# Performance work log

Measured on AMD Instinct MI355X. Metric: run time of the kernel, lower is better.

## Reference

```python
import jax, jax.numpy as jnp
import numpy as np

N = 8192  # number of candidates being ranked


def setup_inputs() -> dict:
    key = jax.random.key(0)
    k1, k2 = jax.random.split(key)
    logits = jax.random.normal(k1, (N,), dtype=jnp.float32)
    rankings = jax.random.randint(k2, (N,), 0, N).astype(jnp.int64)
    return {"logits": logits, "rankings": rankings}


def reference(logits, rankings):
    # Vectorized WeightedRankNetLoss:
    #   loss = (1/N) * sum_{i<j, r_i<r_j} log(1 + exp(logits[j]-logits[i])) / (r_i + r_j)
    n = logits.shape[0]
    idx = jnp.arange(n)
    # pair selected iff i < j AND rankings[i] < rankings[j]
    pair_mask = (idx[:, None] < idx[None, :]) & (rankings[:, None] < rankings[None, :])
    r = rankings.astype(logits.dtype)
    rsum = r[:, None] + r[None, :]
    # For selected pairs r_j >= r_i + 1 >= 1, so rsum >= 1; clamp only protects masked entries.
    w = jnp.where(pair_mask, 1.0, 0.0) / jnp.maximum(rsum, 1.0)  # [N, N]
    d = logits[None, :] - logits[:, None]  # d[i, j] = logits[j] - logits[i]
    loss = jnp.sum(w * jax.nn.softplus(d))  # softplus = log(1+exp(.)), numerically stable
    return loss / n
```

## Files before the change

### kernel.cpp

```cpp
#include <hip/hip_runtime.h>

#define N_CAND 8192
#define TILE   64
#define NTILES (N_CAND / TILE)
#define NLIVE  (NTILES * (NTILES + 1) / 2)
#define WPB    4
#define NBLK   (NLIVE / WPB)

__device__ __forceinline__ float readlane_f(float x, int lane) {
    return __int_as_float(__builtin_amdgcn_readlane(__float_as_int(x), lane));
}

__global__ __launch_bounds__(256, 8) void ranknet_pairs_kernel(
    const float* __restrict__ logits,
    const int*   __restrict__ rankings,
    float*       __restrict__ partials)
{
    const int lane = threadIdx.x & 63;
    const int wave = threadIdx.x >> 6;
    const int t = __builtin_amdgcn_readfirstlane((int)blockIdx.x * WPB + wave);

    int bj = (int)((__builtin_sqrtf(8.0f * (float)t + 1.0f) - 1.0f) * 0.5f);
    while ((bj + 1) * (bj + 2) / 2 <= t) ++bj;
    while (bj * (bj + 1) / 2 > t)       --bj;
    const int bi = t - bj * (bj + 1) / 2;

    const float LOG2E = 1.4426950408889634f;
    const float INF   = __builtin_inff();

    const float lis = logits[bi * TILE + lane] * LOG2E;
    const float ri  = (float)rankings[bi * TILE + lane];
    const float ljs = logits[bj * TILE + lane] * LOG2E;
    const float rjv = (float)rankings[bj * TILE + lane];

    const float Ei  = __builtin_amdgcn_exp2f(lis);
    const float Ejv = __builtin_amdgcn_exp2f(ljs);

    float accL0 = 0.0f, accL1 = 0.0f, accL2 = 0.0f, accL3 = 0.0f;
    float accW0 = 0.0f, accW1 = 0.0f, accW2 = 0.0f, accW3 = 0.0f;

    if (bi != bj) {
        #pragma unroll
        for (int jj = 0; jj < TILE; jj += 4) {
            const float Ej0 = readlane_f(Ejv, jj    ), rj0 = readlane_f(rjv, jj    );
            const float Ej1 = readlane_f(Ejv, jj + 1), rj1 = readlane_f(rjv, jj + 1);
            const float Ej2 = readlane_f(Ejv, jj + 2), rj2 = readlane_f(rjv, jj + 2);
            const float Ej3 = readlane_f(Ejv, jj + 3), rj3 = readlane_f(rjv, jj + 3);

            const float L0 = __builtin_amdgcn_logf(Ei + Ej0);
            const float L1 = __builtin_amdgcn_logf(Ei + Ej1);
            const float L2 = __builtin_amdgcn_logf(Ei + Ej2);
            const float L3 = __builtin_amdgcn_logf(Ei + Ej3);

            const float rs0 = (rj0 > ri) ? (ri + rj0) : INF;
            const float rs1 = (rj1 > ri) ? (ri + rj1) : INF;
            const float rs2 = (rj2 > ri) ? (ri + rj2) : INF;
            const float rs3 = (rj3 > ri) ? (ri + rj3) : INF;

            const float w0 = __builtin_amdgcn_rcpf(rs0);
            const float w1 = __builtin_amdgcn_rcpf(rs1);
            const float w2 = __builtin_amdgcn_rcpf(rs2);
            const float w3 = __builtin_amdgcn_rcpf(rs3);

            accL0 = fmaf(w0, L0, accL0);  accW0 += w0;
            accL1 = fmaf(w1, L1, accL1);  accW1 += w1;
            accL2 = fmaf(w2, L2, accL2);  accW2 += w2;
            accL3 = fmaf(w3, L3, accL3);  accW3 += w3;
        }
    } else {
        #pragma unroll
        for (int jj = 0; jj < TILE; jj += 4) {
            const float Ej0 = readlane_f(Ejv, jj    ), rj0 = readlane_f(rjv, jj    );
            const float Ej1 = readlane_f(Ejv, jj + 1), rj1 = readlane_f(rjv, jj + 1);
            const float Ej2 = readlane_f(Ejv, jj + 2), rj2 = readlane_f(rjv, jj + 2);
            const float Ej3 = readlane_f(Ejv, jj + 3), rj3 = readlane_f(rjv, jj + 3);

            const float L0 = __builtin_amdgcn_logf(Ei + Ej0);
            const float L1 = __builtin_amdgcn_logf(Ei + Ej1);
            const float L2 = __builtin_amdgcn_logf(Ei + Ej2);
            const float L3 = __builtin_amdgcn_logf(Ei + Ej3);

            const float rs0 = ((jj     > lane) && (rj0 > ri)) ? (ri + rj0) : INF;
            const float rs1 = ((jj + 1 > lane) && (rj1 > ri)) ? (ri + rj1) : INF;
            const float rs2 = ((jj + 2 > lane) && (rj2 > ri)) ? (ri + rj2) : INF;
            const float rs3 = ((jj + 3 > lane) && (rj3 > ri)) ? (ri + rj3) : INF;

            const float w0 = __builtin_amdgcn_rcpf(rs0);
            const float w1 = __builtin_amdgcn_rcpf(rs1);
            const float w2 = __builtin_amdgcn_rcpf(rs2);
            const float w3 = __builtin_amdgcn_rcpf(rs3);

            accL0 = fmaf(w0, L0, accL0);  accW0 += w0;
            accL1 = fmaf(w1, L1, accL1);  accW1 += w1;
            accL2 = fmaf(w2, L2, accL2);  accW2 += w2;
            accL3 = fmaf(w3, L3, accL3);  accW3 += w3;
        }
    }

    const float accL = (accL0 + accL1) + (accL2 + accL3);
    const float accW = (accW0 + accW1) + (accW2 + accW3);
    float acc = fmaf(-lis, accW, accL);
    #pragma unroll
    for (int off = 32; off > 0; off >>= 1)
        acc += __shfl_down(acc, off, 64);
    if (lane == 0)
        partials[t] = acc;
}

__global__ __launch_bounds__(1024) void ranknet_reduce_kernel(
    const float* __restrict__ partials,
    float*       __restrict__ out)
{
    __shared__ float s_part[16];
    const int tid = threadIdx.x;

    float acc = 0.0f;
    for (int k = tid; k < NLIVE; k += 1024)
        acc += partials[k];

    #pragma unroll
    for (int off = 32; off > 0; off >>= 1)
        acc += __shfl_down(acc, off, 64);
    if ((tid & 63) == 0) s_part[tid >> 6] = acc;
    __syncthreads();
    if (tid == 0) {
        float s = 0.0f;
        #pragma unroll
        for (int w = 0; w < 16; ++w) s += s_part[w];
        const float LN2 = 0.6931471805599453f;
        out[0] = s * (LN2 / (float)N_CAND);
    }
}

extern "C" void kernel_launch(void* const* d_in, const int* in_sizes, int n_in,
                              void* d_out, int out_size, void* d_ws, size_t ws_size,
                              hipStream_t stream)
{
    const float* logits   = (const float*)d_in[0];
    const int*   rankings = (const int*)  d_in[1];
    float*       out      = (float*)d_out;
    float*       partials = (float*)d_ws;

    ranknet_pairs_kernel<<<dim3(NBLK), dim3(256), 0, stream>>>(logits, rankings, partials);
    ranknet_reduce_kernel<<<1, 1024, 0, stream>>>(partials, out);
}
```

Measured before the change: 69.86 us.

## Use persistent fixed grid with two tiles per wave and split remainder tiles

Replaces one-tile-per-wave launch with a fixed grid of 1024 blocks where each wave processes two full tiles. The 64 leftover tiles are split into 16-column chunks assigned to a subset of waves. Partials are reduced per block in shared memory, so the final reduction reads one value per thread. The inner loops are no longer unrolled, which adds loop and dynamic readlane overhead in exchange for the smaller code size.

Result: no change. 70.39 us (+0.8%).

```diff
diff --git a/kernel.cpp b/kernel.cpp
--- a/kernel.cpp
+++ b/kernel.cpp
@@ -5,21 +5,18 @@
 #define NTILES (N_CAND / TILE)
 #define NLIVE  (NTILES * (NTILES + 1) / 2)
 #define WPB    4
-#define NBLK   (NLIVE / WPB)
+#define NBLK   1024
+#define NWAVE  (NBLK * WPB)
 
 __device__ __forceinline__ float readlane_f(float x, int lane) {
     return __int_as_float(__builtin_amdgcn_readlane(__float_as_int(x), lane));
 }
 
-__global__ __launch_bounds__(256, 8) void ranknet_pairs_kernel(
-    const float* __restrict__ logits,
-    const int*   __restrict__ rankings,
-    float*       __restrict__ partials)
+__device__ __forceinline__ float tile_range_sum(const float* __restrict__ logits,
+                                                const int*   __restrict__ rankings,
+                                                int t, int lane, int j0, int j1)
 {
-    const int lane = threadIdx.x & 63;
-    const int wave = threadIdx.x >> 6;
-    const int t = __builtin_amdgcn_readfirstlane((int)blockIdx.x * WPB + wave);
-
+    t = __builtin_amdgcn_readfirstlane(t);
     int bj = (int)((__builtin_sqrtf(8.0f * (float)t + 1.0f) - 1.0f) * 0.5f);
     while ((bj + 1) * (bj + 2) / 2 <= t) ++bj;
     while (bj * (bj + 1) / 2 > t)       --bj;
@@ -40,8 +37,8 @@
     float accW0 = 0.0f, accW1 = 0.0f, accW2 = 0.0f, accW3 = 0.0f;
 
     if (bi != bj) {
-        #pragma unroll
-        for (int jj = 0; jj < TILE; jj += 4) {
+        #pragma unroll 1
+        for (int jj = j0; jj < j1; jj += 4) {
             const float Ej0 = readlane_f(Ejv, jj    ), rj0 = readlane_f(rjv, jj    );
             const float Ej1 = readlane_f(Ejv, jj + 1), rj1 = readlane_f(rjv, jj + 1);
             const float Ej2 = readlane_f(Ejv, jj + 2), rj2 = readlane_f(rjv, jj + 2);
@@ -68,8 +65,8 @@
             accL3 = fmaf(w3, L3, accL3);  accW3 += w3;
         }
     } else {
-        #pragma unroll
-        for (int jj = 0; jj < TILE; jj += 4) {
+        #pragma unroll 1
+        for (int jj = j0; jj < j1; jj += 4) {
             const float Ej0 = readlane_f(Ejv, jj    ), rj0 = readlane_f(rjv, jj    );
             const float Ej1 = readlane_f(Ejv, jj + 1), rj1 = readlane_f(rjv, jj + 1);
             const float Ej2 = readlane_f(Ejv, jj + 2), rj2 = readlane_f(rjv, jj + 2);
@@ -99,12 +96,44 @@
 
     const float accL = (accL0 + accL1) + (accL2 + accL3);
     const float accW = (accW0 + accW1) + (accW2 + accW3);
-    float acc = fmaf(-lis, accW, accL);
+    return fmaf(-lis, accW, accL);
+}
+
+__global__ __launch_bounds__(256, 4) void ranknet_pairs_kernel(
+    const float* __restrict__ logits,
+    const int*   __restrict__ rankings,
+    float*       __restrict__ partials)
+{
+    const int lane = threadIdx.x & 63;
+    const int wave = threadIdx.x >> 6;
+    const int gw   = __builtin_amdgcn_readfirstlane((int)blockIdx.x * WPB + wave);
+
+    float lacc = 0.0f;
+    #pragma unroll 1
+    for (int k = 0; k < 3; ++k) {
+        int tt, jj0, jj1;
+        bool live = true;
+        if (k == 0)      { tt = gw;          jj0 = 0; jj1 = TILE; }
+        else if (k == 1) { tt = gw + NWAVE;  jj0 = 0; jj1 = TILE; }
+        else {
+            const int c = gw >> 4;
+            live = ((gw & 15) == (c & 3));
+            tt   = 2 * NWAVE + (c >> 2);
+            jj0  = (c & 3) * 16;
+            jj1  = jj0 + 16;
+        }
+        if (live) lacc += tile_range_sum(logits, rankings, tt, lane, jj0, jj1);
+    }
+
     #pragma unroll
     for (int off = 32; off > 0; off >>= 1)
-        acc += __shfl_down(acc, off, 64);
-    if (lane == 0)
-        partials[t] = acc;
+        lacc += __shfl_down(lacc, off, 64);
+
+    __shared__ float s_w[WPB];
+    if (lane == 0) s_w[wave] = lacc;
+    __syncthreads();
+    if (threadIdx.x == 0)
+        partials[blockIdx.x] = (s_w[0] + s_w[1]) + (s_w[2] + s_w[3]);
 }
 
 __global__ __launch_bounds__(1024) void ranknet_reduce_kernel(
@@ -114,9 +143,7 @@
     __shared__ float s_part[16];
     const int tid = threadIdx.x;
 
-    float acc = 0.0f;
-    for (int k = tid; k < NLIVE; k += 1024)
-        acc += partials[k];
+    float acc = partials[tid];
 
     #pragma unroll
     for (int off = 32; off > 0; off >>= 1)
```
